# Kernel tuning notes

Measured on AMD Instinct MI355X. Metric: run time of the kernel, lower is better.

The kernel has to match this reference:

```python
import jax, jax.numpy as jnp
import numpy as np

ALPHA = 0.2  # LeakyReLU negative slope

def setup_inputs() -> dict:
    key = jax.random.key(0)
    kx, kw, kb, ka = jax.random.split(key, 4)
    B, K, D, H = 4, 256, 128, 4
    x = jax.random.normal(kx, (B, K, D), dtype=jnp.float32)
    # Per-head Linear(2D -> D): stored as (H, 2D, D), i.e. transposed torch layout (y = v @ W + b)
    W = jax.random.normal(kw, (H, 2 * D, D), dtype=jnp.float32) * (1.0 / np.sqrt(2 * D))
    lin_b = jax.random.normal(kb, (H, D), dtype=jnp.float32) * 0.01
    # Per-head attention vector a: (H, D)
    a = jax.random.normal(ka, (H, D), dtype=jnp.float32) * (1.0 / np.sqrt(D))
    # Per-head additive bias over attention logits, initialized to zeros like the torch module
    bias = jnp.zeros((H, K, K), dtype=jnp.float32)
    return {"x": x, "W": W, "lin_b": lin_b, "a": a, "bias": bias}

def reference(x, W, lin_b, a, bias):
    # GATv2, dense all-pairs attention over K nodes, eval mode (dropout off).
    # Faithful decomposition: Linear(concat(x_i, x_j)) == x_i @ W_src + x_j @ W_dst + b
    B, K, D = x.shape
    H = W.shape[0]
    outs = []
    for h in range(H):  # small fixed head count; each head has distinct params
        W_src, W_dst = W[h, :D], W[h, D:]          # (D, D) each
        left = x @ W_src                            # (B, K, D) -> contribution of node i
        right = x @ W_dst                           # (B, K, D) -> contribution of node j
        s = left[:, :, None, :] + right[:, None, :, :] + lin_b[h]  # (B, K, K, D)
        s = jnp.where(s > 0, s, ALPHA * s)          # LeakyReLU
        e = jnp.einsum('bijd,d->bij', s, a[h]) + bias[h]           # (B, K, K)
        attn = jax.nn.softmax(e, axis=2)
        outs.append(attn @ x)                       # (B, K, D)
    return jnp.mean(jnp.stack(outs, axis=-1), axis=-1)
```

## Files before the change

kernel.cpp:

```cpp
#include <hip/hip_runtime.h>
#include <math.h>

constexpr int Kc = 256, Dc = 128, Mc = 1024;

typedef _Float16 h2_t __attribute__((ext_vector_type(2)));
union U32H2 { unsigned int u; h2_t h; };
__device__ inline h2_t u2h(unsigned int u) { U32H2 x; x.u = u; return x.h; }
__device__ inline unsigned int h2u(h2_t h) { U32H2 x; x.h = h; return x.u; }
__device__ inline unsigned int packh(float a, float b) {
    h2_t h; h.x = (_Float16)a; h.y = (_Float16)b; return h2u(h);
}

#if __has_builtin(__builtin_amdgcn_fdot2)
__device__ inline float dot2h(unsigned int a, unsigned int b, float c) {
    return __builtin_amdgcn_fdot2(u2h(a), u2h(b), c, false);
}
#else
__device__ inline float dot2h(unsigned int a, unsigned int b, float c) {
    h2_t ah = u2h(a), bh = u2h(b);
    return fmaf((float)ah.x, (float)bh.x, fmaf((float)ah.y, (float)bh.y, c));
}
#endif

__device__ inline float estep(unsigned int r, unsigned int l, h2_t av, float acc) {
    h2_t s = u2h(r) + u2h(l);
    unsigned int t = h2u(s) & 0x7FFF7FFFu;
#if __has_builtin(__builtin_amdgcn_fdot2)
    return __builtin_amdgcn_fdot2(u2h(t), av, acc, false);
#else
    h2_t th = u2h(t);
    return fmaf((float)th.x, (float)av.x, fmaf((float)th.y, (float)av.y, acc));
#endif
}

__global__ __launch_bounds__(256) void k1(const float* __restrict__ x,
                                          const float* __restrict__ W,
                                          const float* __restrict__ lin_b,
                                          const float* __restrict__ a,
                                          unsigned int* __restrict__ Lpp,
                                          unsigned int* __restrict__ Rtp,
                                          float* __restrict__ eb) {
    __shared__ unsigned int As2[64 * 64];
    __shared__ unsigned int Bs2[64 * 64];
    __shared__ float red[4][16][4];

    const int tid = threadIdx.x;
    const int bid = blockIdx.x;
    const int tx = tid & 15, ty = tid >> 4;
    const bool isL = (bid < 128);

    int h, b, m0, n0, dt;
    if (isL) {
        const int nt = bid & 1, mt = (bid >> 1) & 15;
        h = (bid >> 5) & 3; b = 0; dt = 0;
        m0 = mt * 64; n0 = nt * 64;
        {
            const int m_l = tid & 63, kq = tid >> 6;
            #pragma unroll
            for (int c = 0; c < 8; ++c) {
                const float4 v = *(const float4*)&x[(m0 + m_l) * Dc + kq * 32 + c * 4];
                As2[(kq * 16 + c * 2 + 0) * 64 + m_l] = packh(v.x, v.y);
                As2[(kq * 16 + c * 2 + 1) * 64 + m_l] = packh(v.z, v.w);
            }
        }
        {
            const int n_l = tid & 63, kq = tid >> 6;
            const float* Wb = W + (h * 2) * Dc * Dc;
            #pragma unroll
            for (int kk = 0; kk < 16; ++kk) {
                const int k2 = kq * 16 + kk;
                Bs2[k2 * 64 + n_l] =
                    packh(Wb[(2 * k2) * Dc + n0 + n_l], Wb[(2 * k2 + 1) * Dc + n0 + n_l]);
            }
        }
    } else {
        const int r_ = bid - 128;
        const int jt = r_ & 3;
        dt = (r_ >> 2) & 1;
        b  = (r_ >> 3) & 3;
        h  = (r_ >> 5) & 3;
        m0 = dt * 64;
        n0 = jt * 64;
        {
            const int d_l = tid & 63, kq = tid >> 6;
            const float* Wb = W + ((h * 2 + 1) * Dc) * Dc;
            #pragma unroll
            for (int kk = 0; kk < 16; ++kk) {
                const int k2 = kq * 16 + kk;
                As2[k2 * 64 + d_l] =
                    packh(Wb[(2 * k2) * Dc + m0 + d_l], Wb[(2 * k2 + 1) * Dc + m0 + d_l]);
            }
        }
        {
            const int j_l = tid & 63, kq = tid >> 6;
            #pragma unroll
            for (int c = 0; c < 8; ++c) {
                const float4 v = *(const float4*)&x[(b * Kc + n0 + j_l) * Dc + kq * 32 + c * 4];
                Bs2[(kq * 16 + c * 2 + 0) * 64 + j_l] = packh(v.x, v.y);
                Bs2[(kq * 16 + c * 2 + 1) * 64 + j_l] = packh(v.z, v.w);
            }
        }
    }
    __syncthreads();

    float acc[4][4];
    #pragma unroll
    for (int r = 0; r < 4; ++r)
        #pragma unroll
        for (int c = 0; c < 4; ++c) acc[r][c] = 0.f;

    #pragma unroll 8
    for (int k2 = 0; k2 < 64; ++k2) {
        const uint4 xa = *(const uint4*)&As2[k2 * 64 + ty * 4];
        const uint4 wb = *(const uint4*)&Bs2[k2 * 64 + tx * 4];
        acc[0][0] = dot2h(xa.x, wb.x, acc[0][0]);
        acc[0][1] = dot2h(xa.x, wb.y, acc[0][1]);
        acc[0][2] = dot2h(xa.x, wb.z, acc[0][2]);
        acc[0][3] = dot2h(xa.x, wb.w, acc[0][3]);
        acc[1][0] = dot2h(xa.y, wb.x, acc[1][0]);
        acc[1][1] = dot2h(xa.y, wb.y, acc[1][1]);
        acc[1][2] = dot2h(xa.y, wb.z, acc[1][2]);
        acc[1][3] = dot2h(xa.y, wb.w, acc[1][3]);
        acc[2][0] = dot2h(xa.z, wb.x, acc[2][0]);
        acc[2][1] = dot2h(xa.z, wb.y, acc[2][1]);
        acc[2][2] = dot2h(xa.z, wb.z, acc[2][2]);
        acc[2][3] = dot2h(xa.z, wb.w, acc[2][3]);
        acc[3][0] = dot2h(xa.w, wb.x, acc[3][0]);
        acc[3][1] = dot2h(xa.w, wb.y, acc[3][1]);
        acc[3][2] = dot2h(xa.w, wb.z, acc[3][2]);
        acc[3][3] = dot2h(xa.w, wb.w, acc[3][3]);
    }

    if (isL) {
        const float4 lv = *(const float4*)&lin_b[h * Dc + n0 + tx * 4];
        #pragma unroll
        for (int r = 0; r < 4; ++r) {
            uint2 pk;
            pk.x = packh(acc[r][0] + lv.x, acc[r][1] + lv.y);
            pk.y = packh(acc[r][2] + lv.z, acc[r][3] + lv.w);
            *(uint2*)&Lpp[(h * Mc + m0 + ty * 4 + r) * 64 + (n0 >> 1) + tx * 2] = pk;
        }
    } else {
        #pragma unroll
        for (int rp = 0; rp < 2; ++rp) {
            uint4 pk;
            pk.x = packh(acc[2 * rp][0], acc[2 * rp + 1][0]);
            pk.y = packh(acc[2 * rp][1], acc[2 * rp + 1][1]);
            pk.z = packh(acc[2 * rp][2], acc[2 * rp + 1][2]);
            pk.w = packh(acc[2 * rp][3], acc[2 * rp + 1][3]);
            *(uint4*)&Rtp[((h * 4 + b) * 64 + (m0 >> 1) + ty * 2 + rp) * Kc + n0 + tx * 4] = pk;
        }
        const float4 av = *(const float4*)&a[h * Dc + m0 + ty * 4];
        float p0 = 0.4f * (av.x * acc[0][0] + av.y * acc[1][0] + av.z * acc[2][0] + av.w * acc[3][0]);
        float p1 = 0.4f * (av.x * acc[0][1] + av.y * acc[1][1] + av.z * acc[2][1] + av.w * acc[3][1]);
        float p2 = 0.4f * (av.x * acc[0][2] + av.y * acc[1][2] + av.z * acc[2][2] + av.w * acc[3][2]);
        float p3 = 0.4f * (av.x * acc[0][3] + av.y * acc[1][3] + av.z * acc[2][3] + av.w * acc[3][3]);
        p0 += __shfl_xor(p0, 16, 64); p0 += __shfl_xor(p0, 32, 64);
        p1 += __shfl_xor(p1, 16, 64); p1 += __shfl_xor(p1, 32, 64);
        p2 += __shfl_xor(p2, 16, 64); p2 += __shfl_xor(p2, 32, 64);
        p3 += __shfl_xor(p3, 16, 64); p3 += __shfl_xor(p3, 32, 64);
        if (((tid >> 4) & 3) == 0) {
            const int w = tid >> 6;
            red[w][tx][0] = p0; red[w][tx][1] = p1;
            red[w][tx][2] = p2; red[w][tx][3] = p3;
        }
        __syncthreads();
        if (tid < 64) {
            const int txl = tid >> 2, c = tid & 3;
            const float v = red[0][txl][c] + red[1][txl][c] + red[2][txl][c] + red[3][txl][c];
            eb[((h * 4 + b) * 2 + dt) * Kc + n0 + tid] = 1.5f * v;
        }
    }
}

#define E4(ACC, LPV)                               \
    ACC.x = estep(rr.x, LPV, av, ACC.x);           \
    ACC.y = estep(rr.y, LPV, av, ACC.y);           \
    ACC.z = estep(rr.z, LPV, av, ACC.z);           \
    ACC.w = estep(rr.w, LPV, av, ACC.w);

__global__ __launch_bounds__(256) void k2(const float* __restrict__ x,
                                          const float* __restrict__ a,
                                          const float* __restrict__ bias,
                                          const unsigned int* __restrict__ Lpp,
                                          const unsigned int* __restrict__ Rtp,
                                          const float* __restrict__ eb,
                                          float* __restrict__ out) {
    __shared__ float red[256 * 12];
    __shared__ unsigned int lpT2[4 * 64 * 2];
    __shared__ unsigned int aa2s[4 * 64];
    __shared__ float plbar[2 * Kc];

    const int tid = threadIdx.x;
    const int L = blockIdx.x;
    const int xcd = L & 7;
    const int b = xcd >> 1;
    const int it = ((L >> 3) << 1) | (xcd & 1);
    const int i0 = it * 2;

    {
        const int h = tid >> 6, dp = tid & 63;
        uint2 v;
        v.x = Lpp[(h * Mc + b * Kc + i0 + 0) * 64 + dp];
        v.y = Lpp[(h * Mc + b * Kc + i0 + 1) * 64 + dp];
        *(uint2*)&lpT2[(h * 64 + dp) * 2] = v;
        aa2s[tid] = packh(0.4f * a[h * Dc + 2 * dp], 0.4f * a[h * Dc + 2 * dp + 1]);
    }
    if (tid < 128) ((float4*)plbar)[tid] = make_float4(0.f, 0.f, 0.f, 0.f);
    __syncthreads();

    const int dq = tid >> 6, j4 = tid & 63;
    const int w = tid >> 6, l = tid & 63;

    #pragma unroll 1
    for (int h = 0; h < 4; ++h) {
        const int hb = h * 4 + b;
        float4 acc0 = make_float4(0.f, 0.f, 0.f, 0.f);
        float4 acc1 = make_float4(0.f, 0.f, 0.f, 0.f);
        {
            const unsigned int* rb = Rtp + (hb * 64 + dq * 16) * Kc + j4 * 4;
            const unsigned int* lt = lpT2 + (h * 64 + dq * 16) * 2;
            const unsigned int* at = aa2s + h * 64 + dq * 16;
            #pragma unroll
            for (int dp = 0; dp < 16; ++dp) {
                const uint4 rr = *(const uint4*)(rb + dp * Kc);
                const uint2 lp2 = *(const uint2*)(lt + dp * 2);
                const h2_t av = u2h(at[dp]);
                E4(acc0, lp2.x);
                E4(acc1, lp2.y);
            }
        }
        {
            float* myred = red + tid * 12;
            *(float4*)&myred[0] = acc0;
            *(float4*)&myred[4] = acc1;
        }
        __syncthreads();

        if (w < 2) {
            float4 e0 = make_float4(0.f, 0.f, 0.f, 0.f);
            #pragma unroll
            for (int q4 = 0; q4 < 4; ++q4) {
                const float4 v = *(const float4*)&red[(q4 * 64 + l) * 12 + w * 4];
                e0.x += v.x; e0.y += v.y; e0.z += v.z; e0.w += v.w;
            }
            float4 ebs;
            {
                const float4 v0 = *(const float4*)&eb[(hb * 2 + 0) * Kc + l * 4];
                const float4 v1 = *(const float4*)&eb[(hb * 2 + 1) * Kc + l * 4];
                ebs.x = v0.x + v1.x; ebs.y = v0.y + v1.y;
                ebs.z = v0.z + v1.z; ebs.w = v0.w + v1.w;
            }
            const float4 bv = *(const float4*)&bias[(h * Kc + i0 + w) * Kc + l * 4];
            e0.x += ebs.x + bv.x;
            e0.y += ebs.y + bv.y;
            e0.z += ebs.z + bv.z;
            e0.w += ebs.w + bv.w;

            float m = fmaxf(fmaxf(e0.x, e0.y), fmaxf(e0.z, e0.w));
            #pragma unroll
            for (int off = 1; off < 64; off <<= 1) m = fmaxf(m, __shfl_xor(m, off, 64));
            const float p0 = __expf(e0.x - m), p1 = __expf(e0.y - m);
            const float p2 = __expf(e0.z - m), p3 = __expf(e0.w - m);
            float s = p0 + p1 + p2 + p3;
            #pragma unroll
            for (int off = 1; off < 64; off <<= 1) s += __shfl_xor(s, off, 64);
            const float sc = 0.25f / s;
            float4 cur = *(float4*)&plbar[w * Kc + l * 4];
            cur.x = fmaf(p0, sc, cur.x);
            cur.y = fmaf(p1, sc, cur.y);
            cur.z = fmaf(p2, sc, cur.z);
            cur.w = fmaf(p3, sc, cur.w);
            *(float4*)&plbar[w * Kc + l * 4] = cur;
        }
        __syncthreads();
    }

    const int jq = tid >> 5, dd4 = tid & 31;
    float4 o0 = make_float4(0.f, 0.f, 0.f, 0.f);
    float4 o1 = make_float4(0.f, 0.f, 0.f, 0.f);
    {
        const float* xb = x + (b * Kc) * Dc + dd4 * 4;
        #pragma unroll 4
        for (int jj = 0; jj < 32; ++jj) {
            const int j = jj * 8 + jq;
            const float4 xv = *(const float4*)(xb + j * Dc);
            const float pv0 = plbar[j];
            const float pv1 = plbar[Kc + j];
            o0.x = fmaf(pv0, xv.x, o0.x); o0.y = fmaf(pv0, xv.y, o0.y);
            o0.z = fmaf(pv0, xv.z, o0.z); o0.w = fmaf(pv0, xv.w, o0.w);
            o1.x = fmaf(pv1, xv.x, o1.x); o1.y = fmaf(pv1, xv.y, o1.y);
            o1.z = fmaf(pv1, xv.z, o1.z); o1.w = fmaf(pv1, xv.w, o1.w);
        }
    }
    {
        float* myred = red + (jq * 32 + dd4) * 12;
        *(float4*)&myred[0] = o0;
        *(float4*)&myred[4] = o1;
    }
    __syncthreads();
    if (tid < 64) {
        const int i_f = tid >> 5, dd_f = tid & 31;
        float4 s = make_float4(0.f, 0.f, 0.f, 0.f);
        #pragma unroll
        for (int q = 0; q < 8; ++q) {
            const float4 v = *(const float4*)&red[(q * 32 + dd_f) * 12 + i_f * 4];
            s.x += v.x; s.y += v.y; s.z += v.z; s.w += v.w;
        }
        *(float4*)&out[(b * Kc + i0 + i_f) * Dc + dd_f * 4] = s;
    }
}

extern "C" void kernel_launch(void* const* d_in, const int* in_sizes, int n_in,
                              void* d_out, int out_size, void* d_ws, size_t ws_size,
                              hipStream_t stream) {
    const float* x     = (const float*)d_in[0];
    const float* W     = (const float*)d_in[1];
    const float* lin_b = (const float*)d_in[2];
    const float* a     = (const float*)d_in[3];
    const float* bias  = (const float*)d_in[4];
    float* out = (float*)d_out;

    unsigned int*   Lpp = (unsigned int*)d_ws;
    unsigned int*   Rtp = Lpp + 4 * Mc * 64;
    float*          eb  = (float*)(Rtp + 16 * 64 * Kc);

    k1<<<256, 256, 0, stream>>>(x, W, lin_b, a, Lpp, Rtp, eb);
    k2<<<512, 256, 0, stream>>>(x, a, bias, Lpp, Rtp, eb, out);
}
```

Baseline: 25.19 us.

## Assign one head per wavefront and compute all heads concurrently

Result: faster. 23.53 us (-6.6%).

```diff
diff --git a/kernel.cpp b/kernel.cpp
--- a/kernel.cpp
+++ b/kernel.cpp
@@ -199,82 +199,89 @@
     const int i0 = it * 2;
 
     {
-        const int h = tid >> 6, dp = tid & 63;
+        const int hs = tid >> 6, dp = tid & 63;
         uint2 v;
-        v.x = Lpp[(h * Mc + b * Kc + i0 + 0) * 64 + dp];
-        v.y = Lpp[(h * Mc + b * Kc + i0 + 1) * 64 + dp];
-        *(uint2*)&lpT2[(h * 64 + dp) * 2] = v;
-        aa2s[tid] = packh(0.4f * a[h * Dc + 2 * dp], 0.4f * a[h * Dc + 2 * dp + 1]);
-    }
-    if (tid < 128) ((float4*)plbar)[tid] = make_float4(0.f, 0.f, 0.f, 0.f);
-    __syncthreads();
-
-    const int dq = tid >> 6, j4 = tid & 63;
-    const int w = tid >> 6, l = tid & 63;
-
-    #pragma unroll 1
-    for (int h = 0; h < 4; ++h) {
-        const int hb = h * 4 + b;
-        float4 acc0 = make_float4(0.f, 0.f, 0.f, 0.f);
-        float4 acc1 = make_float4(0.f, 0.f, 0.f, 0.f);
-        {
-            const unsigned int* rb = Rtp + (hb * 64 + dq * 16) * Kc + j4 * 4;
-            const unsigned int* lt = lpT2 + (h * 64 + dq * 16) * 2;
-            const unsigned int* at = aa2s + h * 64 + dq * 16;
-            #pragma unroll
-            for (int dp = 0; dp < 16; ++dp) {
-                const uint4 rr = *(const uint4*)(rb + dp * Kc);
-                const uint2 lp2 = *(const uint2*)(lt + dp * 2);
-                const h2_t av = u2h(at[dp]);
-                E4(acc0, lp2.x);
-                E4(acc1, lp2.y);
-            }
-        }
-        {
-            float* myred = red + tid * 12;
-            *(float4*)&myred[0] = acc0;
-            *(float4*)&myred[4] = acc1;
-        }
-        __syncthreads();
-
-        if (w < 2) {
-            float4 e0 = make_float4(0.f, 0.f, 0.f, 0.f);
-            #pragma unroll
-            for (int q4 = 0; q4 < 4; ++q4) {
-                const float4 v = *(const float4*)&red[(q4 * 64 + l) * 12 + w * 4];
-                e0.x += v.x; e0.y += v.y; e0.z += v.z; e0.w += v.w;
-            }
-            float4 ebs;
-            {
-                const float4 v0 = *(const float4*)&eb[(hb * 2 + 0) * Kc + l * 4];
-                const float4 v1 = *(const float4*)&eb[(hb * 2 + 1) * Kc + l * 4];
-                ebs.x = v0.x + v1.x; ebs.y = v0.y + v1.y;
-                ebs.z = v0.z + v1.z; ebs.w = v0.w + v1.w;
-            }
-            const float4 bv = *(const float4*)&bias[(h * Kc + i0 + w) * Kc + l * 4];
-            e0.x += ebs.x + bv.x;
-            e0.y += ebs.y + bv.y;
-            e0.z += ebs.z + bv.z;
-            e0.w += ebs.w + bv.w;
-
-            float m = fmaxf(fmaxf(e0.x, e0.y), fmaxf(e0.z, e0.w));
+        v.x = Lpp[(hs * Mc + b * Kc + i0 + 0) * 64 + dp];
+        v.y = Lpp[(hs * Mc + b * Kc + i0 + 1) * 64 + dp];
+        *(uint2*)&lpT2[(hs * 64 + dp) * 2] = v;
+        aa2s[tid] = packh(0.4f * a[hs * Dc + 2 * dp], 0.4f * a[hs * Dc + 2 * dp + 1]);
+    }
+    __syncthreads();
+
+    const int h = tid >> 6, j4 = tid & 63;
+    const int hb = h * 4 + b;
+
+    float4 acc0 = make_float4(0.f, 0.f, 0.f, 0.f);
+    float4 acc1 = make_float4(0.f, 0.f, 0.f, 0.f);
+    {
+        const unsigned int* rb = Rtp + (hb * 64) * Kc + j4 * 4;
+        const unsigned int* lt = lpT2 + (h * 64) * 2;
+        const unsigned int* at = aa2s + h * 64;
+        #pragma unroll 8
+        for (int dp = 0; dp < 64; ++dp) {
+            const uint4 rr = *(const uint4*)(rb + dp * Kc);
+            const uint2 lp2 = *(const uint2*)(lt + dp * 2);
+            const h2_t av = u2h(at[dp]);
+            E4(acc0, lp2.x);
+            E4(acc1, lp2.y);
+        }
+    }
+
+    {
+        float4 ebs;
+        {
+            const float4 v0 = *(const float4*)&eb[(hb * 2 + 0) * Kc + j4 * 4];
+            const float4 v1 = *(const float4*)&eb[(hb * 2 + 1) * Kc + j4 * 4];
+            ebs.x = v0.x + v1.x; ebs.y = v0.y + v1.y;
+            ebs.z = v0.z + v1.z; ebs.w = v0.w + v1.w;
+        }
+        const float4 bv0 = *(const float4*)&bias[(h * Kc + i0 + 0) * Kc + j4 * 4];
+        const float4 bv1 = *(const float4*)&bias[(h * Kc + i0 + 1) * Kc + j4 * 4];
+        acc0.x += ebs.x + bv0.x; acc0.y += ebs.y + bv0.y;
+        acc0.z += ebs.z + bv0.z; acc0.w += ebs.w + bv0.w;
+        acc1.x += ebs.x + bv1.x; acc1.y += ebs.y + bv1.y;
+        acc1.z += ebs.z + bv1.z; acc1.w += ebs.w + bv1.w;
+
+        {
+            float m = fmaxf(fmaxf(acc0.x, acc0.y), fmaxf(acc0.z, acc0.w));
             #pragma unroll
             for (int off = 1; off < 64; off <<= 1) m = fmaxf(m, __shfl_xor(m, off, 64));
-            const float p0 = __expf(e0.x - m), p1 = __expf(e0.y - m);
-            const float p2 = __expf(e0.z - m), p3 = __expf(e0.w - m);
+            const float p0 = __expf(acc0.x - m), p1 = __expf(acc0.y - m);
+            const float p2 = __expf(acc0.z - m), p3 = __expf(acc0.w - m);
             float s = p0 + p1 + p2 + p3;
             #pragma unroll
             for (int off = 1; off < 64; off <<= 1) s += __shfl_xor(s, off, 64);
             const float sc = 0.25f / s;
-            float4 cur = *(float4*)&plbar[w * Kc + l * 4];
-            cur.x = fmaf(p0, sc, cur.x);
-            cur.y = fmaf(p1, sc, cur.y);
-            cur.z = fmaf(p2, sc, cur.z);
-            cur.w = fmaf(p3, sc, cur.w);
-            *(float4*)&plbar[w * Kc + l * 4] = cur;
-        }
-        __syncthreads();
-    }
+            *(float4*)&red[h * 512 + 0 * Kc + j4 * 4] =
+                make_float4(p0 * sc, p1 * sc, p2 * sc, p3 * sc);
+        }
+        {
+            float m = fmaxf(fmaxf(acc1.x, acc1.y), fmaxf(acc1.z, acc1.w));
+            #pragma unroll
+            for (int off = 1; off < 64; off <<= 1) m = fmaxf(m, __shfl_xor(m, off, 64));
+            const float p0 = __expf(acc1.x - m), p1 = __expf(acc1.y - m);
+            const float p2 = __expf(acc1.z - m), p3 = __expf(acc1.w - m);
+            float s = p0 + p1 + p2 + p3;
+            #pragma unroll
+            for (int off = 1; off < 64; off <<= 1) s += __shfl_xor(s, off, 64);
+            const float sc = 0.25f / s;
+            *(float4*)&red[h * 512 + 1 * Kc + j4 * 4] =
+                make_float4(p0 * sc, p1 * sc, p2 * sc, p3 * sc);
+        }
+    }
+    __syncthreads();
+
+    if (tid < 128) {
+        const int r = tid >> 6, c = tid & 63;
+        float4 s = make_float4(0.f, 0.f, 0.f, 0.f);
+        #pragma unroll
+        for (int w4 = 0; w4 < 4; ++w4) {
+            const float4 v = *(const float4*)&red[w4 * 512 + r * Kc + c * 4];
+            s.x += v.x; s.y += v.y; s.z += v.z; s.w += v.w;
+        }
+        *(float4*)&plbar[r * Kc + c * 4] = s;
+    }
+    __syncthreads();
 
     const int jq = tid >> 5, dd4 = tid & 31;
     float4 o0 = make_float4(0.f, 0.f, 0.f, 0.f);
```
